# Optimization experiments

Hardware: AMD Instinct MI355X
Metric: run time of the kernel (lower is better)

Reference implementation:

```python
import jax, jax.numpy as jnp
import numpy as np

M, D, K = 65536, 64, 4096
BETA = 0.25
INIT_STD = 0.1


def setup_inputs() -> dict:
    key = jax.random.key(0)
    k1, k2, k3 = jax.random.split(key, 3)
    z_e = jax.random.normal(k1, (M, D), dtype=jnp.float32)
    codebook_weight = jax.random.normal(k2, (K, D), dtype=jnp.float32) * INIT_STD
    ema_cluster_size = jax.random.uniform(k3, (K,), dtype=jnp.float32)
    return {"z_e": z_e, "codebook_weight": codebook_weight,
            "ema_cluster_size": ema_cluster_size}


def reference(z_e, codebook_weight, ema_cluster_size):
    # Squared-distance matrix: ||z||^2 + ||e||^2 - 2 z.e   -> (M, K)
    z2 = jnp.sum(z_e * z_e, axis=1, keepdims=True)            # (M, 1)
    e2 = jnp.sum(codebook_weight * codebook_weight, axis=1)[None, :]  # (1, K)
    ze = z_e @ codebook_weight.T                               # (M, K)
    dist = z2 + e2 - 2.0 * ze
    indices = jnp.argmin(dist, axis=1)                         # (M,)
    z_q = codebook_weight[indices]                             # (M, D)

    # use_ema=True path (eval mode: no EMA buffer update)
    commit_loss = jnp.mean((z_e - jax.lax.stop_gradient(z_q)) ** 2)
    vq_loss = BETA * commit_loss

    # Straight-through estimator
    z_q_st = z_e + jax.lax.stop_gradient(z_q - z_e)

    # Perplexity from EMA cluster-size buffer
    probs = ema_cluster_size + 1e-10
    probs = probs / jnp.sum(probs)
    perplexity = jnp.exp(-jnp.sum(probs * jnp.log(probs)))
    perplexity = jax.lax.stop_gradient(perplexity)

    return z_q_st, indices, vq_loss, perplexity, z_q
```

## Files before the change

kernel.cpp:

```cpp
#include <hip/hip_runtime.h>
#include <cmath>

#define M_ROWS  65536
#define D_DIM   64
#define K_CODES 4096

#define OFF_IDX  4194304
#define OFF_SCAL 4259840
#define OFF_ZQ   4259842

#define IMG_OFF   (4u << 20)
#define CANDB_OFF 17039368u

#define CH_BYTES 16384
#define CH_QUADS 1024
#define NSPLIT   4
#define NCHB     8

typedef _Float16 f16x8 __attribute__((ext_vector_type(8)));
typedef __attribute__((ext_vector_type(4))) float f32x4;
typedef unsigned long long u64;

__device__ __forceinline__ unsigned short f2h(float f) {
  _Float16 h = (_Float16)f;
  return __builtin_bit_cast(unsigned short, h);
}
__device__ __forceinline__ float h2f(unsigned short u) {
  return (float)__builtin_bit_cast(_Float16, u);
}
__device__ __forceinline__ unsigned int umin_(unsigned int a, unsigned int b) {
  return a < b ? a : b;
}
__device__ __forceinline__ unsigned int med3_u32(unsigned int a, unsigned int b, unsigned int c) {
  unsigned int d;
  asm("v_med3_u32 %0, %1, %2, %3" : "=v"(d) : "v"(a), "v"(b), "v"(c));
  return d;
}

__device__ __forceinline__ void gload_lds16(const void* g, void* l) {
  __builtin_amdgcn_global_load_lds((const __attribute__((address_space(1))) void*)g,
                                   (__attribute__((address_space(3))) void*)l, 16, 0, 0);
}
__device__ __forceinline__ void gload_lds4(const void* g, void* l) {
  __builtin_amdgcn_global_load_lds((const __attribute__((address_space(1))) void*)g,
                                   (__attribute__((address_space(3))) void*)l, 4, 0, 0);
}

__device__ __forceinline__ float exact_dist(const float4* z4, float z2,
                                            const float* __restrict__ cb,
                                            const float* __restrict__ e2, int k) {
  const float4* ev = (const float4*)(cb + (size_t)k * 64);
  float4 a0 = make_float4(0.f, 0.f, 0.f, 0.f);
  float4 a1 = make_float4(0.f, 0.f, 0.f, 0.f);
  float4 a2 = make_float4(0.f, 0.f, 0.f, 0.f);
  float4 a3 = make_float4(0.f, 0.f, 0.f, 0.f);
#pragma unroll
  for (int q = 0; q < 4; ++q) {
    float4 e0 = ev[4 * q + 0], e1 = ev[4 * q + 1], e2v = ev[4 * q + 2], e3 = ev[4 * q + 3];
    a0.x = fmaf(z4[4 * q + 0].x, e0.x, a0.x); a0.y = fmaf(z4[4 * q + 0].y, e0.y, a0.y);
    a0.z = fmaf(z4[4 * q + 0].z, e0.z, a0.z); a0.w = fmaf(z4[4 * q + 0].w, e0.w, a0.w);
    a1.x = fmaf(z4[4 * q + 1].x, e1.x, a1.x); a1.y = fmaf(z4[4 * q + 1].y, e1.y, a1.y);
    a1.z = fmaf(z4[4 * q + 1].z, e1.z, a1.z); a1.w = fmaf(z4[4 * q + 1].w, e1.w, a1.w);
    a2.x = fmaf(z4[4 * q + 2].x, e2v.x, a2.x); a2.y = fmaf(z4[4 * q + 2].y, e2v.y, a2.y);
    a2.z = fmaf(z4[4 * q + 2].z, e2v.z, a2.z); a2.w = fmaf(z4[4 * q + 2].w, e2v.w, a2.w);
    a3.x = fmaf(z4[4 * q + 3].x, e3.x, a3.x); a3.y = fmaf(z4[4 * q + 3].y, e3.y, a3.y);
    a3.z = fmaf(z4[4 * q + 3].z, e3.z, a3.z); a3.w = fmaf(z4[4 * q + 3].w, e3.w, a3.w);
  }
  float d;
  {
#pragma clang fp contract(off)
    float sx = (a0.x + a1.x) + (a2.x + a3.x);
    float sy = (a0.y + a1.y) + (a2.y + a3.y);
    float sz = (a0.z + a1.z) + (a2.z + a3.z);
    float sw = (a0.w + a1.w) + (a2.w + a3.w);
    float dot = (sx + sy) + (sz + sw);
    float tt = z2 + e2[k];
    d = tt - 2.0f * dot;
  }
  return d;
}

__device__ __forceinline__ float exact_z2(const float4* z4) {
#pragma clang fp contract(off)
  float rr[8];
  {
    const float* f = (const float*)&z4[0];
#pragma unroll
    for (int j = 0; j < 8; ++j) rr[j] = f[j] * f[j];
  }
#pragma unroll
  for (int a = 1; a < 8; ++a) {
    const float* f = (const float*)&z4[2 * a];
#pragma unroll
    for (int j = 0; j < 8; ++j) rr[j] = rr[j] + f[j] * f[j];
  }
  return ((rr[0] + rr[1]) + (rr[2] + rr[3])) + ((rr[4] + rr[5]) + (rr[6] + rr[7]));
}

__global__ void prep_kernel(const float* __restrict__ cb, char* __restrict__ img,
                            float* __restrict__ e2, float* __restrict__ e2b) {
  int t = blockIdx.x * 256 + threadIdx.x;
  {
    int k  = t >> 4;
    int d0 = (t & 15) * 4;
    float4 f = ((const float4*)cb)[t];
    ushort4 hi;
    hi.x = f2h(f.x);
    hi.y = f2h(f.y);
    hi.z = f2h(f.z);
    hi.w = f2h(f.w);
    int c = k >> 7, r = k & 127;
    int g = d0 >> 3;
    int off = ((g + r) & 7) * 16 + (d0 & 7) * 2;
    char* base = img + (size_t)c * CH_BYTES + r * 128;
    *(ushort4*)(base + off) = hi;
  }
  if (t < K_CODES) {
    const float4* row = (const float4*)(cb + (size_t)t * D_DIM);
    float4 q[16];
#pragma unroll
    for (int i = 0; i < 16; ++i) q[i] = row[i];
    float s = exact_z2(q);
    e2[t] = s;
    e2b[t] = s + 32.0f;
  }
}

__global__ __launch_bounds__(512, 4)
void vq_mfma_kernel(const float* __restrict__ z_e,
                    const char* __restrict__ img,
                    const float* __restrict__ e2b,
                    u64* __restrict__ cand64) {
  __shared__ union {
    uint4 q[2][CH_QUADS];
    char raw[2][CH_BYTES];
    unsigned int cand[256 * 33];
  } sm;
  __shared__ float lds_e2[2][128];
  const int tid  = threadIdx.x;
  const int wave = tid >> 6, lane = tid & 63;
  const int quad = lane >> 4, c16 = lane & 15;
  const int rb   = blockIdx.x >> 2;
  const int sp   = blockIdx.x & 3;
  const int mb   = rb * 512 + wave * 64;

  {
    const uint4* src = (const uint4*)(img + (size_t)(sp * NCHB + 0) * CH_BYTES);
    gload_lds16(src + tid, &sm.q[0][tid]);
    gload_lds16(src + tid + 512, &sm.q[0][tid + 512]);
    if (tid < 128) gload_lds4(e2b + sp * 1024 + 0 * 128 + tid, &lds_e2[0][tid]);
  }

  f16x8 zh[4][2];
#pragma unroll
  for (int mt = 0; mt < 4; ++mt) {
    int m = mb + mt * 16 + c16;
#pragma unroll
    for (int s = 0; s < 2; ++s) {
      const float* zp = z_e + (size_t)m * 64 + s * 32 + quad * 8;
      float4 fa = ((const float4*)zp)[0];
      float4 fb = ((const float4*)zp)[1];
      float v[8] = {fa.x, fa.y, fa.z, fa.w, fb.x, fb.y, fb.z, fb.w};
      union { f16x8 v8; unsigned short e[8]; } H;
#pragma unroll
      for (int j = 0; j < 8; ++j) H.e[j] = f2h(-2.0f * v[j]);
      zh[mt][s] = H.v8;
    }
  }

  unsigned int b1[4][4], b2[4][4];
#pragma unroll
  for (int mt = 0; mt < 4; ++mt)
#pragma unroll
    for (int r = 0; r < 4; ++r) { b1[mt][r] = 0xFFFFFFFFu; b2[mt][r] = 0xFFFFFFFFu; }

  const int swz0 = ((quad + c16) & 7) * 16;
  const int swz1 = ((quad + 4 + c16) & 7) * 16;

  __syncthreads();

  int cur = 0;
  for (int c = 0; c < NCHB; ++c) {
    if (c + 1 < NCHB) {
      const int nb = cur ^ 1;
      const uint4* src = (const uint4*)(img + (size_t)(sp * NCHB + c + 1) * CH_BYTES);
      gload_lds16(src + tid, &sm.q[nb][tid]);
      gload_lds16(src + tid + 512, &sm.q[nb][tid + 512]);
      if (tid < 128) gload_lds4(e2b + sp * 1024 + (c + 1) * 128 + tid, &lds_e2[nb][tid]);
    }

#pragma unroll 1
    for (int t = 0; t < 8; ++t) {
      const char* hb = sm.raw[cur] + (t * 16 + c16) * 128;
      f16x8 Bh0 = *(const f16x8*)(hb + swz0);
      f16x8 Bh1 = *(const f16x8*)(hb + swz1);
      float e2v = lds_e2[cur][t * 16 + c16];
      unsigned int tid8 = (unsigned int)(sp * 64 + c * 8 + t);
      f32x4 cvec = {e2v, e2v, e2v, e2v};

#pragma unroll
      for (int mt = 0; mt < 4; ++mt) {
        f32x4 acc;
        acc = __builtin_amdgcn_mfma_f32_16x16x32_f16(zh[mt][0], Bh0, cvec, 0, 0, 0);
        acc = __builtin_amdgcn_mfma_f32_16x16x32_f16(zh[mt][1], Bh1, acc, 0, 0, 0);
#pragma unroll
        for (int r = 0; r < 4; ++r) {
          unsigned int key = (__float_as_uint(acc[r]) & 0xFFFFFF00u) | tid8;
          b2[mt][r] = med3_u32(b1[mt][r], b2[mt][r], key);
          b1[mt][r] = umin_(b1[mt][r], key);
        }
      }
    }
    __syncthreads();
    cur ^= 1;
  }

  for (int pass = 0; pass < 2; ++pass) {
    __syncthreads();
    if ((wave >> 2) == pass) {
      int wl = wave & 3;
#pragma unroll
      for (int mt = 0; mt < 4; ++mt)
#pragma unroll
        for (int r = 0; r < 4; ++r) {
          int lr = wl * 64 + mt * 16 + quad * 4 + r;
          sm.cand[lr * 33 + c16 * 2 + 0] = b1[mt][r];
          sm.cand[lr * 33 + c16 * 2 + 1] = b2[mt][r];
        }
    }
    __syncthreads();
    if (tid < 256) {
      unsigned int kk[4] = {0xFFFFFFFFu, 0xFFFFFFFFu, 0xFFFFFFFFu, 0xFFFFFFFFu};
      unsigned int vv[4] = {0, 0, 0, 0};
      for (int j = 0; j < 32; ++j) {
        unsigned int key = sm.cand[tid * 33 + j];
        if (key < kk[3]) {
          kk[3] = key;
          vv[3] = (key & 0xFFu) * 16 + (unsigned int)(j >> 1);
          for (int p = 3; p > 0; --p)
            if (kk[p] < kk[p - 1]) {
              unsigned int a = kk[p]; kk[p] = kk[p - 1]; kk[p - 1] = a;
              unsigned int b = vv[p]; vv[p] = vv[p - 1]; vv[p - 1] = b;
            }
        }
      }
      int grow = rb * 512 + pass * 256 + tid;
#pragma unroll
      for (int i = 0; i < 4; ++i)
        cand64[(size_t)grow * 16 + sp * 4 + i] = ((u64)kk[i] << 32) | (u64)vv[i];
    }
  }
}

__global__ __launch_bounds__(256)
void pick_kernel(const float* __restrict__ z_e, const float* __restrict__ cb,
                 const float* __restrict__ e2, const u64* __restrict__ cand64,
                 float* __restrict__ out) {
  __shared__ int list[256];
  __shared__ int lcnt;
  const int tid = threadIdx.x;
  const int r   = blockIdx.x * 256 + tid;
  if (tid == 0) lcnt = 0;
  __syncthreads();

  u64 m1 = ~0ull, m2 = ~0ull;
#pragma unroll 4
  for (int j = 0; j < 16; ++j) {
    u64 v = cand64[(size_t)r * 16 + j];
    if (v < m1) { m2 = m1; m1 = v; }
    else if (v < m2) m2 = v;
  }

  unsigned int key1 = (unsigned int)(m1 >> 32) & 0xFFFFFF00u;
  unsigned int key2 = (unsigned int)(m2 >> 32) & 0xFFFFFF00u;
  bool ambig = (key2 - key1) < 2048u;
  if (!ambig) {
    out[OFF_IDX + r] = (float)(unsigned int)(m1 & 0xFFFFFFFFu);
  } else {
    list[atomicAdd(&lcnt, 1)] = tid;
  }
  __syncthreads();

  int n = lcnt;
  if (tid < n) {
    int rr = blockIdx.x * 256 + list[tid];
    const float4* zr = (const float4*)(z_e + (size_t)rr * 64);
    float4 z4[16];
#pragma unroll
    for (int j = 0; j < 16; ++j) z4[j] = zr[j];
    float z2 = exact_z2(z4);

    float bd = INFINITY;
    int bk = K_CODES;
#pragma unroll 1
    for (int ci = 0; ci < 16; ++ci) {
      int k = (int)(unsigned int)(cand64[(size_t)rr * 16 + ci] & 0xFFFFFFFFu);
      float d = exact_dist(z4, z2, cb, e2, k);
      if (d < bd || (d == bd && k < bk)) { bd = d; bk = k; }
    }
    out[OFF_IDX + rr] = (float)bk;
  }
}

__global__ __launch_bounds__(256)
void zq_kernel(const float* __restrict__ z_e, const float* __restrict__ cb,
               float* __restrict__ out, double* __restrict__ partials) {
  const int tid = threadIdx.x;
  const int t   = blockIdx.x * 256 + tid;
  const int m   = t >> 4, seg = t & 15;

  int k = (int)out[OFF_IDX + m];
  float4 q = *(const float4*)(cb + (size_t)k * 64 + seg * 4);
  float4 z = *(const float4*)(z_e + (size_t)m * 64 + seg * 4);

  ((float4*)out)[(size_t)m * 16 + seg] = q;
  float* d1 = out + OFF_ZQ + (size_t)m * 64 + seg * 4;
  ((float2*)d1)[0] = make_float2(q.x, q.y);
  ((float2*)d1)[1] = make_float2(q.z, q.w);

  float dx = z.x - q.x, dy = z.y - q.y, dz = z.z - q.z, dw = z.w - q.w;
  double csum = (double)dx * dx + (double)dy * dy + (double)dz * dz + (double)dw * dw;
#pragma unroll
  for (int off = 32; off > 0; off >>= 1) csum += __shfl_down(csum, off);
  if ((tid & 63) == 0) partials[blockIdx.x * 4 + (tid >> 6)] = csum;
}

__global__ void finalize_kernel(const float* __restrict__ ema,
                                const double* __restrict__ partials,
                                float* __restrict__ out) {
  __shared__ double red[1024];
  const int t = threadIdx.x;

  double cs = 0.0;
  for (int i = t; i < 16384; i += 1024) cs += partials[i];
  red[t] = cs;
  __syncthreads();
  for (int off = 512; off > 0; off >>= 1) {
    if (t < off) red[t] += red[t + off];
    __syncthreads();
  }
  double commit = red[0];
  __syncthreads();

  double s = 0.0;
  for (int i = t; i < K_CODES; i += 1024) s += (double)(ema[i] + 1e-10f);
  red[t] = s;
  __syncthreads();
  for (int off = 512; off > 0; off >>= 1) {
    if (t < off) red[t] += red[t + off];
    __syncthreads();
  }
  double S = red[0];
  __syncthreads();

  double h = 0.0;
  for (int i = t; i < K_CODES; i += 1024) {
    float p = (float)((ema[i] + 1e-10f) / (float)S);
    h += (double)(p * logf(p));
  }
  red[t] = h;
  __syncthreads();
  for (int off = 512; off > 0; off >>= 1) {
    if (t < off) red[t] += red[t + off];
    __syncthreads();
  }

  if (t == 0) {
    out[OFF_SCAL]     = 0.25f * (float)(commit / (double)((size_t)M_ROWS * (size_t)D_DIM));
    out[OFF_SCAL + 1] = expf((float)(-red[0]));
  }
}

extern "C" void kernel_launch(void* const* d_in, const int* in_sizes, int n_in,
                              void* d_out, int out_size, void* d_ws, size_t ws_size,
                              hipStream_t stream) {
  (void)in_sizes; (void)n_in; (void)out_size;
  const float* z_e = (const float*)d_in[0];
  const float* cb  = (const float*)d_in[1];
  const float* ema = (const float*)d_in[2];
  float* out = (float*)d_out;

  float*  e2       = (float*)d_ws;
  float*  e2b      = (float*)((char*)d_ws + 16384);
  double* partials = (double*)((char*)d_ws + 32768);
  char*   img      = (char*)d_out + IMG_OFF;

  const size_t cand_bytes = (size_t)M_ROWS * 16 * 8;
  const int use_ws = (ws_size >= 163840 + cand_bytes) ? 1 : 0;
  u64* cand64 = use_ws
      ? (u64*)((char*)d_ws + 163840)
      : (u64*)((char*)d_out + CANDB_OFF);

  prep_kernel<<<(K_CODES * D_DIM / 4) / 256, 256, 0, stream>>>(cb, img, e2, e2b);
  vq_mfma_kernel<<<(M_ROWS / 512) * NSPLIT, 512, 0, stream>>>(z_e, img, e2b, cand64);
  pick_kernel<<<M_ROWS / 256, 256, 0, stream>>>(z_e, cb, e2, cand64, out);
  zq_kernel<<<M_ROWS * 16 / 256, 256, 0, stream>>>(z_e, cb, out, partials);
  finalize_kernel<<<1, 1024, 0, stream>>>(ema, partials, out);
}
```

Before: 169.4 us.

## Fuse candidate pick with z_q gather and parallelize exact rescoring across lanes

Fuses the pick and z_q/commit-loss kernels when the candidate buffer lives in workspace, so the chosen indices stay in shared memory instead of round-tripping through global memory and an extra launch. The candidate scan is split across four lanes per row with shuffle merges. Ambiguous rows are rescored by 16 lanes, one candidate each, combined with a shuffle min over an order-preserving key, instead of one thread looping over 16 candidates. This adds a fallback path and reduces the partials count, at the cost of more block-level synchronization.

```diff
diff --git a/kernel.cpp b/kernel.cpp
--- a/kernel.cpp
+++ b/kernel.cpp
@@ -95,6 +95,11 @@
     for (int j = 0; j < 8; ++j) rr[j] = rr[j] + f[j] * f[j];
   }
   return ((rr[0] + rr[1]) + (rr[2] + rr[3])) + ((rr[4] + rr[5]) + (rr[6] + rr[7]));
+}
+
+__device__ __forceinline__ unsigned int ford(float f) {
+  unsigned int b = __float_as_uint(f);
+  return b ^ ((((int)b) >> 31) | 0x80000000u);
 }
 
 __global__ void prep_kernel(const float* __restrict__ cb, char* __restrict__ img,
@@ -252,54 +257,150 @@
   }
 }
 
+__device__ __forceinline__ void pick_scan4(const u64* __restrict__ cand64,
+                                           int row, int part, u64& s1, u64& s2) {
+  s1 = ~0ull; s2 = ~0ull;
+  const u64* cp = cand64 + (size_t)row * 16 + part * 4;
+#pragma unroll
+  for (int j = 0; j < 4; ++j) {
+    u64 v = cp[j];
+    if (v < s1) { s2 = s1; s1 = v; }
+    else if (v < s2) s2 = v;
+  }
+#pragma unroll
+  for (int m = 1; m <= 2; m <<= 1) {
+    u64 o1 = __shfl_xor(s1, m);
+    u64 o2 = __shfl_xor(s2, m);
+    u64 hi  = s1 > o1 ? s1 : o1;
+    u64 lo2 = s2 < o2 ? s2 : o2;
+    s1 = s1 < o1 ? s1 : o1;
+    s2 = hi < lo2 ? hi : lo2;
+  }
+}
+
+__device__ __forceinline__ int pick_exact16(const float* __restrict__ z_e,
+                                            const float* __restrict__ cb,
+                                            const float* __restrict__ e2,
+                                            const u64* __restrict__ cand64,
+                                            int row, int lane16) {
+  const int k = (int)(unsigned int)(cand64[(size_t)row * 16 + lane16] & 0xFFFFFFFFu);
+  const float4* zr = (const float4*)(z_e + (size_t)row * 64);
+  float4 z4[16];
+#pragma unroll
+  for (int j = 0; j < 16; ++j) z4[j] = zr[j];
+  float z2 = exact_z2(z4);
+  float d = exact_dist(z4, z2, cb, e2, k);
+  u64 kk = ((u64)ford(d) << 32) | (unsigned int)k;
+#pragma unroll
+  for (int m = 1; m <= 8; m <<= 1) {
+    u64 o = __shfl_xor(kk, m);
+    kk = o < kk ? o : kk;
+  }
+  return (int)(unsigned int)(kk & 0xFFFFFFFFu);
+}
+
 __global__ __launch_bounds__(256)
 void pick_kernel(const float* __restrict__ z_e, const float* __restrict__ cb,
                  const float* __restrict__ e2, const u64* __restrict__ cand64,
                  float* __restrict__ out) {
-  __shared__ int list[256];
+  __shared__ int list[64];
   __shared__ int lcnt;
   const int tid = threadIdx.x;
-  const int r   = blockIdx.x * 256 + tid;
+  const int R0  = blockIdx.x * 64;
   if (tid == 0) lcnt = 0;
   __syncthreads();
 
-  u64 m1 = ~0ull, m2 = ~0ull;
-#pragma unroll 4
-  for (int j = 0; j < 16; ++j) {
-    u64 v = cand64[(size_t)r * 16 + j];
-    if (v < m1) { m2 = m1; m1 = v; }
-    else if (v < m2) m2 = v;
-  }
-
-  unsigned int key1 = (unsigned int)(m1 >> 32) & 0xFFFFFF00u;
-  unsigned int key2 = (unsigned int)(m2 >> 32) & 0xFFFFFF00u;
-  bool ambig = (key2 - key1) < 2048u;
-  if (!ambig) {
-    out[OFF_IDX + r] = (float)(unsigned int)(m1 & 0xFFFFFFFFu);
-  } else {
-    list[atomicAdd(&lcnt, 1)] = tid;
-  }
-  __syncthreads();
-
-  int n = lcnt;
-  if (tid < n) {
-    int rr = blockIdx.x * 256 + list[tid];
-    const float4* zr = (const float4*)(z_e + (size_t)rr * 64);
-    float4 z4[16];
-#pragma unroll
-    for (int j = 0; j < 16; ++j) z4[j] = zr[j];
-    float z2 = exact_z2(z4);
-
-    float bd = INFINITY;
-    int bk = K_CODES;
-#pragma unroll 1
-    for (int ci = 0; ci < 16; ++ci) {
-      int k = (int)(unsigned int)(cand64[(size_t)rr * 16 + ci] & 0xFFFFFFFFu);
-      float d = exact_dist(z4, z2, cb, e2, k);
-      if (d < bd || (d == bd && k < bk)) { bd = d; bk = k; }
-    }
-    out[OFF_IDX + rr] = (float)bk;
-  }
+  {
+    const int row = R0 + (tid >> 2);
+    u64 s1, s2;
+    pick_scan4(cand64, row, tid & 3, s1, s2);
+    if ((tid & 3) == 0) {
+      unsigned int key1 = (unsigned int)(s1 >> 32) & 0xFFFFFF00u;
+      unsigned int key2 = (unsigned int)(s2 >> 32) & 0xFFFFFF00u;
+      if ((key2 - key1) >= 2048u) {
+        out[OFF_IDX + row] = (float)(unsigned int)(s1 & 0xFFFFFFFFu);
+      } else {
+        list[atomicAdd(&lcnt, 1)] = row - R0;
+      }
+    }
+  }
+  __syncthreads();
+
+  const int n = lcnt;
+  const int lane16 = tid & 15;
+  for (int g = tid >> 4; g < n; g += 16) {
+    const int row = R0 + list[g];
+    int bk = pick_exact16(z_e, cb, e2, cand64, row, lane16);
+    if (lane16 == 0) out[OFF_IDX + row] = (float)bk;
+  }
+}
+
+__global__ __launch_bounds__(256)
+void pickzq_kernel(const float* __restrict__ z_e, const float* __restrict__ cb,
+                   const float* __restrict__ e2, const u64* __restrict__ cand64,
+                   float* __restrict__ out, double* __restrict__ partials) {
+  __shared__ int sidx[64];
+  __shared__ int list[64];
+  __shared__ int lcnt;
+  __shared__ double red[4];
+  const int tid = threadIdx.x;
+  const int R0  = blockIdx.x * 64;
+  if (tid == 0) lcnt = 0;
+  __syncthreads();
+
+  {
+    const int row = R0 + (tid >> 2);
+    u64 s1, s2;
+    pick_scan4(cand64, row, tid & 3, s1, s2);
+    if ((tid & 3) == 0) {
+      unsigned int key1 = (unsigned int)(s1 >> 32) & 0xFFFFFF00u;
+      unsigned int key2 = (unsigned int)(s2 >> 32) & 0xFFFFFF00u;
+      int lr = row - R0;
+      if ((key2 - key1) >= 2048u) {
+        int k = (int)(unsigned int)(s1 & 0xFFFFFFFFu);
+        sidx[lr] = k;
+        out[OFF_IDX + row] = (float)k;
+      } else {
+        list[atomicAdd(&lcnt, 1)] = lr;
+      }
+    }
+  }
+  __syncthreads();
+
+  {
+    const int n = lcnt;
+    const int lane16 = tid & 15;
+    for (int g = tid >> 4; g < n; g += 16) {
+      const int lr = list[g];
+      int bk = pick_exact16(z_e, cb, e2, cand64, R0 + lr, lane16);
+      if (lane16 == 0) {
+        sidx[lr] = bk;
+        out[OFF_IDX + R0 + lr] = (float)bk;
+      }
+    }
+  }
+  __syncthreads();
+
+  double csum = 0.0;
+#pragma unroll
+  for (int p = 0; p < 4; ++p) {
+    const int m   = R0 + p * 16 + (tid >> 4);
+    const int seg = tid & 15;
+    const int k   = sidx[m - R0];
+    float4 q = *(const float4*)(cb + (size_t)k * 64 + seg * 4);
+    float4 z = *(const float4*)(z_e + (size_t)m * 64 + seg * 4);
+    ((float4*)out)[(size_t)m * 16 + seg] = q;
+    float* d1 = out + OFF_ZQ + (size_t)m * 64 + seg * 4;
+    ((float2*)d1)[0] = make_float2(q.x, q.y);
+    ((float2*)d1)[1] = make_float2(q.z, q.w);
+    float dx = z.x - q.x, dy = z.y - q.y, dz = z.z - q.z, dw = z.w - q.w;
+    csum += (double)dx * dx + (double)dy * dy + (double)dz * dz + (double)dw * dw;
+  }
+#pragma unroll
+  for (int off = 32; off > 0; off >>= 1) csum += __shfl_down(csum, off);
+  if ((tid & 63) == 0) red[tid >> 6] = csum;
+  __syncthreads();
+  if (tid == 0) partials[blockIdx.x] = red[0] + red[1] + red[2] + red[3];
 }
 
 __global__ __launch_bounds__(256)
@@ -326,13 +427,13 @@
 }
 
 __global__ void finalize_kernel(const float* __restrict__ ema,
-                                const double* __restrict__ partials,
+                                const double* __restrict__ partials, int n,
                                 float* __restrict__ out) {
   __shared__ double red[1024];
   const int t = threadIdx.x;
 
   double cs = 0.0;
-  for (int i = t; i < 16384; i += 1024) cs += partials[i];
+  for (int i = t; i < n; i += 1024) cs += partials[i];
   red[t] = cs;
   __syncthreads();
   for (int off = 512; off > 0; off >>= 1) {
@@ -393,7 +494,12 @@
 
   prep_kernel<<<(K_CODES * D_DIM / 4) / 256, 256, 0, stream>>>(cb, img, e2, e2b);
   vq_mfma_kernel<<<(M_ROWS / 512) * NSPLIT, 512, 0, stream>>>(z_e, img, e2b, cand64);
-  pick_kernel<<<M_ROWS / 256, 256, 0, stream>>>(z_e, cb, e2, cand64, out);
-  zq_kernel<<<M_ROWS * 16 / 256, 256, 0, stream>>>(z_e, cb, out, partials);
-  finalize_kernel<<<1, 1024, 0, stream>>>(ema, partials, out);
-}
+  if (use_ws) {
+    pickzq_kernel<<<M_ROWS / 64, 256, 0, stream>>>(z_e, cb, e2, cand64, out, partials);
+    finalize_kernel<<<1, 1024, 0, stream>>>(ema, partials, M_ROWS / 64, out);
+  } else {
+    pick_kernel<<<M_ROWS / 64, 256, 0, stream>>>(z_e, cb, e2, cand64, out);
+    zq_kernel<<<M_ROWS * 16 / 256, 256, 0, stream>>>(z_e, cb, out, partials);
+    finalize_kernel<<<1, 1024, 0, stream>>>(ema, partials, 16384, out);
+  }
+}
```

New measurement: 146.9 us. -13.3%, faster.
